# Performance work log

Hardware: AMD Instinct MI355X
Metric: run time of the kernel (lower is better)

## Reference

```python
import jax, jax.numpy as jnp
import numpy as np

EPS = 1e-12  # matches torch F.normalize eps


def setup_inputs() -> dict:
    key = jax.random.key(0)
    k1, k2, k3 = jax.random.split(key, 3)
    N, C, H, W, K = 16, 1024, 32, 32, 32
    x = jax.random.normal(k1, (N, C, H, W), dtype=jnp.float32)
    # 1x1 conv weight (K, C, 1, 1) stored as (K, C)
    conv_w = jax.random.normal(k2, (K, C), dtype=jnp.float32) * 0.02
    centroids = jax.random.uniform(k3, (K, C), dtype=jnp.float32)
    return {"x": x, "conv_w": conv_w, "centroids": centroids}


def _l2norm(v, axis):
    return v / jnp.maximum(jnp.linalg.norm(v, axis=axis, keepdims=True), EPS)


def reference(x, conv_w, centroids):
    N, C, H, W = x.shape
    K = centroids.shape[0]
    # normalize_input: L2 over channel dim
    x = _l2norm(x, axis=1)
    xf = x.reshape(N, C, H * W)                      # (N, C, P)
    # 1x1 conv == per-pixel matmul -> (N, K, P)
    logits = jnp.einsum('kc,ncp->nkp', conv_w, xf)
    a = jax.nn.softmax(logits, axis=1)               # softmax over clusters
    # sum_p a[n,k,p] * (x[n,:,p] - centroids[k,:])
    # == (a @ x^T) - (sum_p a) * centroids  (two GEMMs, no (N,K,C,P) blowup)
    vlad = jnp.einsum('nkp,ncp->nkc', a, xf) - a.sum(-1)[:, :, None] * centroids[None]
    vlad = _l2norm(vlad, axis=2)                     # intra-cluster L2 norm
    vlad = vlad.reshape(N, K * C)
    vlad = _l2norm(vlad, axis=1)                     # global L2 norm
    return vlad
```

## Files before the change

kernel.cpp:

```cpp
#include <hip/hip_runtime.h>

#define NB   16
#define CC   1024
#define PP   1024
#define KK   32
#define EPSF 1e-12f

typedef __attribute__((ext_vector_type(8))) short  bf16x8;
typedef __attribute__((ext_vector_type(4))) float  f32x4;

__device__ __forceinline__ float bf2f(unsigned short u) {
    union { unsigned int i; float f; } v; v.i = ((unsigned int)u) << 16; return v.f;
}
__device__ __forceinline__ unsigned short f2bf(float f) {
    union { float f; unsigned int i; } v; v.f = f;
    return (unsigned short)((v.i + 0x7fffu + ((v.i >> 16) & 1u)) >> 16);
}

template <typename T> struct IO;
template <> struct IO<float> {
    static __device__ __forceinline__ float  ld (const float* p) { return *p; }
    static __device__ __forceinline__ float4 ld4(const float* p) { return *(const float4*)p; }
};
template <> struct IO<unsigned short> {
    static __device__ __forceinline__ float  ld (const unsigned short* p) { return bf2f(*p); }
    static __device__ __forceinline__ float4 ld4(const unsigned short* p) {
        const ushort4 u = *(const ushort4*)p;
        return make_float4(bf2f(u.x), bf2f(u.y), bf2f(u.z), bf2f(u.w));
    }
};

__global__ __launch_bounds__(256) void k_detect(const unsigned short* __restrict__ xu,
                                                int* __restrict__ flag) {
    __shared__ int s;
    const int t = threadIdx.x;
    if (t == 0) s = 0;
    __syncthreads();
    int bad = 0;
    for (int i = t; i < 4096; i += 256)
        if (((xu[i] >> 7) & 0xFFu) > 0x9Fu) bad = 1;
    if (bad) atomicOr(&s, 1);
    __syncthreads();
    if (t == 0) flag[0] = s;
}

template <typename T>
__device__ __forceinline__ void attn_body(const T* __restrict__ x,
                                          const T* __restrict__ w,
                                          float* __restrict__ rnorm_ws,
                                          unsigned short* __restrict__ attn_g,
                                          float* __restrict__ asum) {
    __shared__ __align__(16) unsigned short xt[32 * 136];
    __shared__ __align__(16) unsigned short w_lds[32 * 136];
    __shared__ float red[32 * 32];
    __shared__ float lg[32 * 33];
    __shared__ float inv_lds[32];
    __shared__ float rnorm_lds[32];
    const int b = blockIdx.x, t = threadIdx.x;
    const int n = b >> 5, pbase = (b & 31) * 32;
    const int lane = t & 63, wv = t >> 6;
    const int quad = lane >> 4, l15 = lane & 15;
    const int mt = wv & 1, nt = wv >> 1;

    const size_t xb = (size_t)n * CC * PP + pbase;
    float ss0 = 0.f, ss1 = 0.f, ss2 = 0.f, ss3 = 0.f;
    f32x4 acc = {0.f, 0.f, 0.f, 0.f};

    const int pxg = 4 * (t & 7);
    const int crow = t >> 3;

    for (int ch = 0; ch < 8; ++ch) {
        const int c0 = ch * 128;
        __syncthreads();
        #pragma unroll
        for (int pass = 0; pass < 4; ++pass) {
            const int cl = crow + 32 * pass;
            const float4 v = IO<T>::ld4(&x[xb + (size_t)(c0 + cl) * PP + pxg]);
            ss0 += v.x * v.x; ss1 += v.y * v.y; ss2 += v.z * v.z; ss3 += v.w * v.w;
            xt[(pxg + 0) * 136 + cl] = f2bf(v.x);
            xt[(pxg + 1) * 136 + cl] = f2bf(v.y);
            xt[(pxg + 2) * 136 + cl] = f2bf(v.z);
            xt[(pxg + 3) * 136 + cl] = f2bf(v.w);
        }
        {
            const int k = t >> 3, cg = (t & 7) * 16;
            #pragma unroll
            for (int j = 0; j < 4; ++j) {
                const float4 v = IO<T>::ld4(&w[k * CC + c0 + cg + 4 * j]);
                ushort4 u;
                u.x = f2bf(v.x); u.y = f2bf(v.y); u.z = f2bf(v.z); u.w = f2bf(v.w);
                *(ushort4*)&w_lds[k * 136 + cg + 4 * j] = u;
            }
        }
        __syncthreads();
        #pragma unroll
        for (int ks = 0; ks < 4; ++ks) {
            const bf16x8 av = *(const bf16x8*)&xt[(mt * 16 + l15) * 136 + ks * 32 + quad * 8];
            const bf16x8 bv = *(const bf16x8*)&w_lds[(nt * 16 + l15) * 136 + ks * 32 + quad * 8];
            acc = __builtin_amdgcn_mfma_f32_16x16x32_bf16(av, bv, acc, 0, 0, 0);
        }
    }
    red[crow * 32 + pxg + 0] = ss0;
    red[crow * 32 + pxg + 1] = ss1;
    red[crow * 32 + pxg + 2] = ss2;
    red[crow * 32 + pxg + 3] = ss3;
    __syncthreads();
    if (t < 32) {
        float s = 0.f;
        #pragma unroll
        for (int g = 0; g < 32; ++g) s += red[g * 32 + t];
        const float r = 1.0f / fmaxf(sqrtf(s), EPSF);
        rnorm_lds[t] = r;
        rnorm_ws[n * PP + pbase + t] = r;
    }
    __syncthreads();
    #pragma unroll
    for (int reg = 0; reg < 4; ++reg) {
        const int px = mt * 16 + quad * 4 + reg;
        lg[px * 33 + nt * 16 + l15] = acc[reg] * rnorm_lds[px];
    }
    __syncthreads();
    if (t < 32) {
        float m = -1e30f;
        #pragma unroll
        for (int k = 0; k < KK; ++k) m = fmaxf(m, lg[t * 33 + k]);
        float s = 0.f;
        #pragma unroll
        for (int k = 0; k < KK; ++k) {
            const float e = expf(lg[t * 33 + k] - m);
            lg[t * 33 + k] = e;
            s += e;
        }
        inv_lds[t] = 1.0f / s;
    }
    __syncthreads();
    {
        const int k = t >> 3;
        float s = 0.f;
        ushort4 u;
        float vv[4];
        #pragma unroll
        for (int j = 0; j < 4; ++j) {
            const int px = pxg + j;
            vv[j] = lg[px * 33 + k] * inv_lds[px];
        }
        u.x = f2bf(vv[0]); u.y = f2bf(vv[1]); u.z = f2bf(vv[2]); u.w = f2bf(vv[3]);
        s = bf2f(u.x) + bf2f(u.y) + bf2f(u.z) + bf2f(u.w);
        *(ushort4*)&attn_g[((size_t)n * KK + k) * PP + pbase + pxg] = u;
        s += __shfl_xor(s, 1, 64);
        s += __shfl_xor(s, 2, 64);
        s += __shfl_xor(s, 4, 64);
        if ((t & 7) == 0) atomicAdd(&asum[n * KK + k], s);
    }
}
__global__ __launch_bounds__(256) void k_attn(const void* __restrict__ x,
                                              const void* __restrict__ w,
                                              const int* __restrict__ flag,
                                              float* __restrict__ rnorm_ws,
                                              unsigned short* __restrict__ attn_g,
                                              float* __restrict__ asum) {
    if (*flag) attn_body<float>((const float*)x, (const float*)w, rnorm_ws, attn_g, asum);
    else       attn_body<unsigned short>((const unsigned short*)x, (const unsigned short*)w,
                                         rnorm_ws, attn_g, asum);
}

template <typename T>
__device__ __forceinline__ void vlad_body(const T* __restrict__ x,
                                          const T* __restrict__ cent,
                                          const float* __restrict__ rnorm_ws,
                                          const unsigned short* __restrict__ attn_g,
                                          const float* __restrict__ asum,
                                          float* __restrict__ vlad,
                                          float* __restrict__ ssqnk) {
    __shared__ __align__(16) unsigned short xt[64 * 136];
    __shared__ __align__(16) unsigned short at_lds[32 * 136];
    __shared__ float asum_lds[32];
    __shared__ float ssq_lds[32];
    const int b = blockIdx.x, t = threadIdx.x;
    const int n = b >> 4, cbase = (b & 15) * 64;
    const int lane = t & 63, wv = t >> 6;
    const int quad = lane >> 4, l15 = lane & 15;
    const int mt = wv & 1, nt0 = (wv >> 1) * 2, nt1 = nt0 + 1;

    if (t < 32) { asum_lds[t] = asum[n * KK + t]; ssq_lds[t] = 0.f; }

    f32x4 acc0 = {0.f, 0.f, 0.f, 0.f}, acc1 = {0.f, 0.f, 0.f, 0.f};
    const size_t xb = (size_t)n * CC * PP + (size_t)cbase * PP;

    for (int pc = 0; pc < 8; ++pc) {
        const int p0 = pc * 128;
        __syncthreads();
        {
            const int k = t >> 3, pg = (t & 7) * 16;
            const size_t base = ((size_t)n * KK + k) * PP + p0 + pg;
            const uint4 u0 = *(const uint4*)&attn_g[base];
            const uint4 u1 = *(const uint4*)&attn_g[base + 8];
            *(uint4*)&at_lds[k * 136 + pg]     = u0;
            *(uint4*)&at_lds[k * 136 + pg + 8] = u1;
        }
        {
            const int pg = 4 * (t & 31);
            const float4 rn = *(const float4*)&rnorm_ws[n * PP + p0 + pg];
            #pragma unroll
            for (int pass = 0; pass < 8; ++pass) {
                const int ci = (t >> 5) + 8 * pass;
                const float4 v = IO<T>::ld4(&x[xb + (size_t)ci * PP + p0 + pg]);
                ushort4 u;
                u.x = f2bf(v.x * rn.x); u.y = f2bf(v.y * rn.y);
                u.z = f2bf(v.z * rn.z); u.w = f2bf(v.w * rn.w);
                *(ushort4*)&xt[ci * 136 + pg] = u;
            }
        }
        __syncthreads();
        #pragma unroll
        for (int ks = 0; ks < 4; ++ks) {
            const bf16x8 av  = *(const bf16x8*)&at_lds[(mt * 16 + l15) * 136 + ks * 32 + quad * 8];
            const bf16x8 bv0 = *(const bf16x8*)&xt[(nt0 * 16 + l15) * 136 + ks * 32 + quad * 8];
            const bf16x8 bv1 = *(const bf16x8*)&xt[(nt1 * 16 + l15) * 136 + ks * 32 + quad * 8];
            acc0 = __builtin_amdgcn_mfma_f32_16x16x32_bf16(av, bv0, acc0, 0, 0, 0);
            acc1 = __builtin_amdgcn_mfma_f32_16x16x32_bf16(av, bv1, acc1, 0, 0, 0);
        }
    }
    __syncthreads();
    const int c0g = cbase + nt0 * 16 + l15, c1g = cbase + nt1 * 16 + l15;
    #pragma unroll
    for (int reg = 0; reg < 4; ++reg) {
        const int k = mt * 16 + quad * 4 + reg;
        const float A = asum_lds[k];
        const float v0 = acc0[reg] - A * IO<T>::ld(&cent[k * CC + c0g]);
        const float v1 = acc1[reg] - A * IO<T>::ld(&cent[k * CC + c1g]);
        vlad[((size_t)n * KK + k) * CC + c0g] = v0;
        vlad[((size_t)n * KK + k) * CC + c1g] = v1;
        float s = v0 * v0 + v1 * v1;
        s += __shfl_xor(s, 1, 64);
        s += __shfl_xor(s, 2, 64);
        s += __shfl_xor(s, 4, 64);
        s += __shfl_xor(s, 8, 64);
        if (l15 == 0) atomicAdd(&ssq_lds[k], s);
    }
    __syncthreads();
    if (t < 32) atomicAdd(&ssqnk[n * KK + t], ssq_lds[t]);
}
__global__ __launch_bounds__(256) void k_vlad(const void* __restrict__ x,
                                              const void* __restrict__ cent,
                                              const int* __restrict__ flag,
                                              const float* __restrict__ rnorm_ws,
                                              const unsigned short* __restrict__ attn_g,
                                              const float* __restrict__ asum,
                                              float* __restrict__ vlad,
                                              float* __restrict__ ssqnk) {
    if (*flag) vlad_body<float>((const float*)x, (const float*)cent, rnorm_ws, attn_g,
                                asum, vlad, ssqnk);
    else       vlad_body<unsigned short>((const unsigned short*)x, (const unsigned short*)cent,
                                         rnorm_ws, attn_g, asum, vlad, ssqnk);
}

__global__ __launch_bounds__(64) void k_factors(const float* __restrict__ ssqnk,
                                                float* __restrict__ rintra,
                                                float* __restrict__ rglob) {
    const int n = blockIdx.x, t = threadIdx.x;
    const float s = (t < KK) ? ssqnk[n * KK + t] : 0.f;
    const float r = 1.0f / fmaxf(sqrtf(s), EPSF);
    if (t < KK) rintra[n * KK + t] = r;
    float g = s * r * r;
    for (int off = 32; off > 0; off >>= 1) g += __shfl_down(g, off, 64);
    if (t == 0) rglob[n] = 1.0f / fmaxf(sqrtf(g), EPSF);
}

__global__ __launch_bounds__(256) void k_out(const float* __restrict__ vlad,
                                             const float* __restrict__ rintra,
                                             const float* __restrict__ rglob,
                                             const int* __restrict__ flag,
                                             void* __restrict__ out) {
    const int b = blockIdx.x, t = threadIdx.x;
    const float f = rintra[b] * rglob[b >> 5];
    const float4 v = ((const float4*)(vlad + (size_t)b * CC))[t];
    if (*flag) {
        float4 o; o.x = v.x * f; o.y = v.y * f; o.z = v.z * f; o.w = v.w * f;
        ((float4*)((float*)out + (size_t)b * CC))[t] = o;
    } else {
        ushort4 u;
        u.x = f2bf(v.x * f); u.y = f2bf(v.y * f);
        u.z = f2bf(v.z * f); u.w = f2bf(v.w * f);
        ((ushort4*)((unsigned short*)out + (size_t)b * CC))[t] = u;
    }
}

extern "C" void kernel_launch(void* const* d_in, const int* in_sizes, int n_in,
                              void* d_out, int out_size, void* d_ws, size_t ws_size,
                              hipStream_t stream) {
    const void* x    = d_in[0];
    const void* w    = d_in[1];
    const void* cent = d_in[2];

    float* ws       = (float*)d_ws;
    float* rnorm_ws = ws;
    float* vlad     = rnorm_ws + NB * PP;
    float* asum     = vlad + NB * KK * CC;
    float* ssqnk    = asum + NB * KK;
    float* rintra   = ssqnk + NB * KK;
    float* rglob    = rintra + NB * KK;
    int*   flag     = (int*)(rglob + NB);
    unsigned short* attn_g = (unsigned short*)(flag + 4);

    hipMemsetAsync(asum, 0, 2 * NB * KK * sizeof(float), stream);

    k_detect<<<1, 256, 0, stream>>>((const unsigned short*)x, flag);
    k_attn<<<NB * 32, 256, 0, stream>>>(x, w, flag, rnorm_ws, attn_g, asum);
    k_vlad<<<NB * 16, 256, 0, stream>>>(x, cent, flag, rnorm_ws, attn_g, asum, vlad, ssqnk);
    k_factors<<<NB, 64, 0, stream>>>(ssqnk, rintra, rglob);
    k_out<<<NB * KK, 256, 0, stream>>>(vlad, rintra, rglob, flag, d_out);
}
```

Measured before the change: 127.6 us.

## Double-buffer LDS with register prefetch, split vlad tiles, fold memset and factors

Both GEMM kernels now prefetch the next chunk of global data into registers and write into alternating LDS buffers, so each iteration needs one barrier instead of two and global loads overlap MFMA work. The vlad kernel halves its channel tile to get twice as many blocks with one accumulator per wave. The memset is folded into the detect kernel and the factors kernel into k_out, which removes two launches. The cost is more register pressure, and the custom barrier relies on lgkmcnt alone for LDS visibility.

Measured after the change: 124.9 us. 2.1% less time.

```diff
diff --git a/kernel.cpp b/kernel.cpp
--- a/kernel.cpp
+++ b/kernel.cpp
@@ -30,10 +30,18 @@
     }
 };
 
+__device__ __forceinline__ void wg_sync_fast() {
+    asm volatile("s_waitcnt lgkmcnt(0)" ::: "memory");
+    __builtin_amdgcn_s_barrier();
+    asm volatile("" ::: "memory");
+}
+
 __global__ __launch_bounds__(256) void k_detect(const unsigned short* __restrict__ xu,
-                                                int* __restrict__ flag) {
+                                                int* __restrict__ flag,
+                                                float* __restrict__ zbuf) {
     __shared__ int s;
     const int t = threadIdx.x;
+    for (int i = t; i < 2 * NB * KK; i += 256) zbuf[i] = 0.f;
     if (t == 0) s = 0;
     __syncthreads();
     int bad = 0;
@@ -50,17 +58,17 @@
                                           float* __restrict__ rnorm_ws,
                                           unsigned short* __restrict__ attn_g,
                                           float* __restrict__ asum) {
-    __shared__ __align__(16) unsigned short xt[32 * 136];
-    __shared__ __align__(16) unsigned short w_lds[32 * 136];
+    __shared__ __align__(16) unsigned short xt[2][32 * 136];
+    __shared__ __align__(16) unsigned short w_lds[2][32 * 136];
     __shared__ float red[32 * 32];
     __shared__ float lg[32 * 33];
     __shared__ float inv_lds[32];
     __shared__ float rnorm_lds[32];
     const int b = blockIdx.x, t = threadIdx.x;
     const int n = b >> 5, pbase = (b & 31) * 32;
-    const int lane = t & 63, wv = t >> 6;
+    const int lane = t & 63, wid = t >> 6;
     const int quad = lane >> 4, l15 = lane & 15;
-    const int mt = wv & 1, nt = wv >> 1;
+    const int mt = wid & 1, nt = wid >> 1;
 
     const size_t xb = (size_t)n * CC * PP + pbase;
     float ss0 = 0.f, ss1 = 0.f, ss2 = 0.f, ss3 = 0.f;
@@ -68,35 +76,50 @@
 
     const int pxg = 4 * (t & 7);
     const int crow = t >> 3;
-
+    const int wcg = (t & 7) * 16;
+
+    float4 xr[4], wr[4];
+    #pragma unroll
+    for (int pass = 0; pass < 4; ++pass)
+        xr[pass] = IO<T>::ld4(&x[xb + (size_t)(crow + 32 * pass) * PP + pxg]);
+    #pragma unroll
+    for (int j = 0; j < 4; ++j)
+        wr[j] = IO<T>::ld4(&w[crow * CC + wcg + 4 * j]);
+
+    #pragma unroll 2
     for (int ch = 0; ch < 8; ++ch) {
-        const int c0 = ch * 128;
-        __syncthreads();
+        const int buf = ch & 1;
         #pragma unroll
         for (int pass = 0; pass < 4; ++pass) {
             const int cl = crow + 32 * pass;
-            const float4 v = IO<T>::ld4(&x[xb + (size_t)(c0 + cl) * PP + pxg]);
+            const float4 v = xr[pass];
             ss0 += v.x * v.x; ss1 += v.y * v.y; ss2 += v.z * v.z; ss3 += v.w * v.w;
-            xt[(pxg + 0) * 136 + cl] = f2bf(v.x);
-            xt[(pxg + 1) * 136 + cl] = f2bf(v.y);
-            xt[(pxg + 2) * 136 + cl] = f2bf(v.z);
-            xt[(pxg + 3) * 136 + cl] = f2bf(v.w);
-        }
-        {
-            const int k = t >> 3, cg = (t & 7) * 16;
+            xt[buf][(pxg + 0) * 136 + cl] = f2bf(v.x);
+            xt[buf][(pxg + 1) * 136 + cl] = f2bf(v.y);
+            xt[buf][(pxg + 2) * 136 + cl] = f2bf(v.z);
+            xt[buf][(pxg + 3) * 136 + cl] = f2bf(v.w);
+        }
+        #pragma unroll
+        for (int j = 0; j < 4; ++j) {
+            const float4 v = wr[j];
+            ushort4 u;
+            u.x = f2bf(v.x); u.y = f2bf(v.y); u.z = f2bf(v.z); u.w = f2bf(v.w);
+            *(ushort4*)&w_lds[buf][crow * 136 + wcg + 4 * j] = u;
+        }
+        if (ch < 7) {
+            const int c0 = (ch + 1) * 128;
             #pragma unroll
-            for (int j = 0; j < 4; ++j) {
-                const float4 v = IO<T>::ld4(&w[k * CC + c0 + cg + 4 * j]);
-                ushort4 u;
-                u.x = f2bf(v.x); u.y = f2bf(v.y); u.z = f2bf(v.z); u.w = f2bf(v.w);
-                *(ushort4*)&w_lds[k * 136 + cg + 4 * j] = u;
-            }
-        }
-        __syncthreads();
+            for (int pass = 0; pass < 4; ++pass)
+                xr[pass] = IO<T>::ld4(&x[xb + (size_t)(c0 + crow + 32 * pass) * PP + pxg]);
+            #pragma unroll
+            for (int j = 0; j < 4; ++j)
+                wr[j] = IO<T>::ld4(&w[crow * CC + c0 + wcg + 4 * j]);
+        }
+        wg_sync_fast();
         #pragma unroll
         for (int ks = 0; ks < 4; ++ks) {
-            const bf16x8 av = *(const bf16x8*)&xt[(mt * 16 + l15) * 136 + ks * 32 + quad * 8];
-            const bf16x8 bv = *(const bf16x8*)&w_lds[(nt * 16 + l15) * 136 + ks * 32 + quad * 8];
+            const bf16x8 av = *(const bf16x8*)&xt[buf][(mt * 16 + l15) * 136 + ks * 32 + quad * 8];
+            const bf16x8 bv = *(const bf16x8*)&w_lds[buf][(nt * 16 + l15) * 136 + ks * 32 + quad * 8];
             acc = __builtin_amdgcn_mfma_f32_16x16x32_bf16(av, bv, acc, 0, 0, 0);
         }
     }
@@ -172,66 +195,76 @@
                                           const float* __restrict__ asum,
                                           float* __restrict__ vlad,
                                           float* __restrict__ ssqnk) {
-    __shared__ __align__(16) unsigned short xt[64 * 136];
-    __shared__ __align__(16) unsigned short at_lds[32 * 136];
+    __shared__ __align__(16) unsigned short xt[2][32 * 136];
+    __shared__ __align__(16) unsigned short at_lds[2][32 * 136];
     __shared__ float asum_lds[32];
     __shared__ float ssq_lds[32];
     const int b = blockIdx.x, t = threadIdx.x;
-    const int n = b >> 4, cbase = (b & 15) * 64;
-    const int lane = t & 63, wv = t >> 6;
+    const int n = b >> 5, cbase = (b & 31) * 32;
+    const int lane = t & 63, wid = t >> 6;
     const int quad = lane >> 4, l15 = lane & 15;
-    const int mt = wv & 1, nt0 = (wv >> 1) * 2, nt1 = nt0 + 1;
+    const int mt = wid & 1, nt = wid >> 1;
 
     if (t < 32) { asum_lds[t] = asum[n * KK + t]; ssq_lds[t] = 0.f; }
 
-    f32x4 acc0 = {0.f, 0.f, 0.f, 0.f}, acc1 = {0.f, 0.f, 0.f, 0.f};
+    f32x4 acc = {0.f, 0.f, 0.f, 0.f};
     const size_t xb = (size_t)n * CC * PP + (size_t)cbase * PP;
 
+    const int ak  = t >> 3, apg = (t & 7) * 16;
+    const int xpg = 4 * (t & 31);
+    const int xc  = t >> 5;
+
+    uint4 a0, a1; float4 xr[4]; float4 rn;
+    {
+        const size_t abase = ((size_t)n * KK + ak) * PP + apg;
+        a0 = *(const uint4*)&attn_g[abase];
+        a1 = *(const uint4*)&attn_g[abase + 8];
+        rn = *(const float4*)&rnorm_ws[n * PP + xpg];
+        #pragma unroll
+        for (int pass = 0; pass < 4; ++pass)
+            xr[pass] = IO<T>::ld4(&x[xb + (size_t)(xc + 8 * pass) * PP + xpg]);
+    }
+
+    #pragma unroll 2
     for (int pc = 0; pc < 8; ++pc) {
-        const int p0 = pc * 128;
-        __syncthreads();
-        {
-            const int k = t >> 3, pg = (t & 7) * 16;
-            const size_t base = ((size_t)n * KK + k) * PP + p0 + pg;
-            const uint4 u0 = *(const uint4*)&attn_g[base];
-            const uint4 u1 = *(const uint4*)&attn_g[base + 8];
-            *(uint4*)&at_lds[k * 136 + pg]     = u0;
-            *(uint4*)&at_lds[k * 136 + pg + 8] = u1;
-        }
-        {
-            const int pg = 4 * (t & 31);
-            const float4 rn = *(const float4*)&rnorm_ws[n * PP + p0 + pg];
+        const int buf = pc & 1;
+        *(uint4*)&at_lds[buf][ak * 136 + apg]     = a0;
+        *(uint4*)&at_lds[buf][ak * 136 + apg + 8] = a1;
+        #pragma unroll
+        for (int pass = 0; pass < 4; ++pass) {
+            const int ci = xc + 8 * pass;
+            const float4 v = xr[pass];
+            ushort4 u;
+            u.x = f2bf(v.x * rn.x); u.y = f2bf(v.y * rn.y);
+            u.z = f2bf(v.z * rn.z); u.w = f2bf(v.w * rn.w);
+            *(ushort4*)&xt[buf][ci * 136 + xpg] = u;
+        }
+        if (pc < 7) {
+            const int p0 = (pc + 1) * 128;
+            const size_t abase = ((size_t)n * KK + ak) * PP + p0 + apg;
+            a0 = *(const uint4*)&attn_g[abase];
+            a1 = *(const uint4*)&attn_g[abase + 8];
+            rn = *(const float4*)&rnorm_ws[n * PP + p0 + xpg];
             #pragma unroll
-            for (int pass = 0; pass < 8; ++pass) {
-                const int ci = (t >> 5) + 8 * pass;
-                const float4 v = IO<T>::ld4(&x[xb + (size_t)ci * PP + p0 + pg]);
-                ushort4 u;
-                u.x = f2bf(v.x * rn.x); u.y = f2bf(v.y * rn.y);
-                u.z = f2bf(v.z * rn.z); u.w = f2bf(v.w * rn.w);
-                *(ushort4*)&xt[ci * 136 + pg] = u;
-            }
-        }
-        __syncthreads();
+            for (int pass = 0; pass < 4; ++pass)
+                xr[pass] = IO<T>::ld4(&x[xb + (size_t)(xc + 8 * pass) * PP + p0 + xpg]);
+        }
+        wg_sync_fast();
         #pragma unroll
         for (int ks = 0; ks < 4; ++ks) {
-            const bf16x8 av  = *(const bf16x8*)&at_lds[(mt * 16 + l15) * 136 + ks * 32 + quad * 8];
-            const bf16x8 bv0 = *(const bf16x8*)&xt[(nt0 * 16 + l15) * 136 + ks * 32 + quad * 8];
-            const bf16x8 bv1 = *(const bf16x8*)&xt[(nt1 * 16 + l15) * 136 + ks * 32 + quad * 8];
-            acc0 = __builtin_amdgcn_mfma_f32_16x16x32_bf16(av, bv0, acc0, 0, 0, 0);
-            acc1 = __builtin_amdgcn_mfma_f32_16x16x32_bf16(av, bv1, acc1, 0, 0, 0);
-        }
-    }
-    __syncthreads();
-    const int c0g = cbase + nt0 * 16 + l15, c1g = cbase + nt1 * 16 + l15;
+            const bf16x8 av = *(const bf16x8*)&at_lds[buf][(mt * 16 + l15) * 136 + ks * 32 + quad * 8];
+            const bf16x8 bv = *(const bf16x8*)&xt[buf][(nt * 16 + l15) * 136 + ks * 32 + quad * 8];
+            acc = __builtin_amdgcn_mfma_f32_16x16x32_bf16(av, bv, acc, 0, 0, 0);
+        }
+    }
+    const int cg = cbase + nt * 16 + l15;
     #pragma unroll
     for (int reg = 0; reg < 4; ++reg) {
         const int k = mt * 16 + quad * 4 + reg;
         const float A = asum_lds[k];
-        const float v0 = acc0[reg] - A * IO<T>::ld(&cent[k * CC + c0g]);
-        const float v1 = acc1[reg] - A * IO<T>::ld(&cent[k * CC + c1g]);
-        vlad[((size_t)n * KK + k) * CC + c0g] = v0;
-        vlad[((size_t)n * KK + k) * CC + c1g] = v1;
-        float s = v0 * v0 + v1 * v1;
+        const float v0 = acc[reg] - A * IO<T>::ld(&cent[k * CC + cg]);
+        vlad[((size_t)n * KK + k) * CC + cg] = v0;
+        float s = v0 * v0;
         s += __shfl_xor(s, 1, 64);
         s += __shfl_xor(s, 2, 64);
         s += __shfl_xor(s, 4, 64);
@@ -255,25 +288,24 @@
                                          rnorm_ws, attn_g, asum, vlad, ssqnk);
 }
 
-__global__ __launch_bounds__(64) void k_factors(const float* __restrict__ ssqnk,
-                                                float* __restrict__ rintra,
-                                                float* __restrict__ rglob) {
-    const int n = blockIdx.x, t = threadIdx.x;
-    const float s = (t < KK) ? ssqnk[n * KK + t] : 0.f;
-    const float r = 1.0f / fmaxf(sqrtf(s), EPSF);
-    if (t < KK) rintra[n * KK + t] = r;
-    float g = s * r * r;
-    for (int off = 32; off > 0; off >>= 1) g += __shfl_down(g, off, 64);
-    if (t == 0) rglob[n] = 1.0f / fmaxf(sqrtf(g), EPSF);
-}
-
 __global__ __launch_bounds__(256) void k_out(const float* __restrict__ vlad,
-                                             const float* __restrict__ rintra,
-                                             const float* __restrict__ rglob,
+                                             const float* __restrict__ ssqnk,
                                              const int* __restrict__ flag,
                                              void* __restrict__ out) {
+    __shared__ float fsh;
     const int b = blockIdx.x, t = threadIdx.x;
-    const float f = rintra[b] * rglob[b >> 5];
+    const int n = b >> 5, k = b & 31;
+    if (t < 64) {
+        const float s = (t < 32) ? ssqnk[n * KK + t] : 0.f;
+        const float r = 1.0f / fmaxf(sqrtf(s), EPSF);
+        float g = s * r * r;
+        #pragma unroll
+        for (int off = 32; off > 0; off >>= 1) g += __shfl_down(g, off, 64);
+        const float rk = __shfl(r, k, 64);
+        if (t == 0) fsh = rk * (1.0f / fmaxf(sqrtf(g), EPSF));
+    }
+    __syncthreads();
+    const float f = fsh;
     const float4 v = ((const float4*)(vlad + (size_t)b * CC))[t];
     if (*flag) {
         float4 o; o.x = v.x * f; o.y = v.y * f; o.z = v.z * f; o.w = v.w * f;
@@ -302,12 +334,10 @@
     float* rglob    = rintra + NB * KK;
     int*   flag     = (int*)(rglob + NB);
     unsigned short* attn_g = (unsigned short*)(flag + 4);
-
-    hipMemsetAsync(asum, 0, 2 * NB * KK * sizeof(float), stream);
-
-    k_detect<<<1, 256, 0, stream>>>((const unsigned short*)x, flag);
+    (void)rintra; (void)rglob;
+
+    k_detect<<<1, 256, 0, stream>>>((const unsigned short*)x, flag, asum);
     k_attn<<<NB * 32, 256, 0, stream>>>(x, w, flag, rnorm_ws, attn_g, asum);
-    k_vlad<<<NB * 16, 256, 0, stream>>>(x, cent, flag, rnorm_ws, attn_g, asum, vlad, ssqnk);
-    k_factors<<<NB, 64, 0, stream>>>(ssqnk, rintra, rglob);
-    k_out<<<NB * KK, 256, 0, stream>>>(vlad, rintra, rglob, flag, d_out);
-}
+    k_vlad<<<NB * 32, 256, 0, stream>>>(x, cent, flag, rnorm_ws, attn_g, asum, vlad, ssqnk);
+    k_out<<<NB * KK, 256, 0, stream>>>(vlad, ssqnk, flag, d_out);
+}
```
